# Kernel tuning notes

Measured on AMD Instinct MI355X. Metric: run time of the kernel, lower is better.

The kernel has to match this reference:

```python
import jax, jax.numpy as jnp
import numpy as np

WAYS, SHOTS = 32, 64
N = WAYS * SHOTS
XDIM, CIN = 84, 3
FLAT = 10 * 19 * 19  # 3610 after conv/pool stack
ZDIM = 2 * 32 * 4    # 256

def _conv2d(x, w, b):
    y = jax.lax.conv_general_dilated(x, w, (1, 1), 'VALID',
        dimension_numbers=('NCHW', 'OIHW', 'NCHW'))
    return y + b[None, :, None, None]

def _maxpool2(x):
    return jax.lax.reduce_window(x, -jnp.inf, jax.lax.max,
        (1, 1, 2, 2), (1, 1, 2, 2), 'VALID')

def setup_inputs() -> dict:
    key = jax.random.key(0)
    ks = jax.random.split(key, 32)
    rn = lambda k, shape, s=0.05: jax.random.normal(k, shape, jnp.float32) * s
    labels = jax.random.randint(ks[0], (N,), 0, WAYS)
    y = jax.nn.one_hot(labels, WAYS, dtype=jnp.float32)
    z = lambda n: jnp.zeros((n,), jnp.float32)
    return {
        'x': jax.random.normal(ks[1], (N, CIN, XDIM, XDIM), jnp.float32),
        'y': y,
        'conv1_w': rn(ks[2], (10, CIN, 3, 3)), 'conv1_b': z(10),
        'conv2_w': rn(ks[3], (10, 10, 3, 3)), 'conv2_b': z(10),
        'enc_w': rn(ks[4], (FLAT, 64)), 'enc_b': z(64),
        't1_w': rn(ks[5], (3, 4), 0.2), 't1_b': z(4),
        'te2_w1': rn(ks[6], (256, 128)), 'te2_b1': z(128),
        'te2_w2': rn(ks[7], (128, 32)), 'te2_b2': z(32),
        't2_w': rn(ks[8], (3, 4), 0.2), 't2_b': z(4),
        'om_mu_w': rn(ks[9], (256, 1)), 'om_mu_b': z(1),
        'om_sd_w': rn(ks[10], (256, 1)), 'om_sd_b': z(1),
        'ga_w': rn(ks[11], (128, 64)), 'ga_b': z(64),
        'ga_mu_w': rn(ks[12], (64, 5)), 'ga_mu_b': z(5),
        'ga_sd_w': rn(ks[13], (64, 5)), 'ga_sd_b': z(5),
        'ze_w': rn(ks[14], (128, 64)), 'ze_b': z(64),
        'ze_mu_w': rn(ks[15], (64, ZDIM)), 'ze_mu_b': z(ZDIM),
        'ze_sd_w': rn(ks[16], (64, ZDIM)), 'ze_sd_b': z(ZDIM),
        'do_sample': 0,
    }

def _kl_std_normal(mu, sigma):
    # KL(N(mu, sigma) || N(0, 1)), summed
    return jnp.sum(-jnp.log(sigma) + 0.5 * (sigma * sigma + mu * mu) - 0.5)

def _forward(x, y, conv1_w, conv1_b, conv2_w, conv2_b, enc_w, enc_b,
             t1_w, t1_b, te2_w1, te2_b1, te2_w2, te2_b2, t2_w, t2_b,
             om_mu_w, om_mu_b, om_sd_w, om_sd_b,
             ga_w, ga_b, ga_mu_w, ga_mu_b, ga_sd_w, ga_sd_b,
             ze_w, ze_b, ze_mu_w, ze_mu_b, ze_sd_w, ze_sd_b):
    relu = jax.nn.relu
    # class encoder: conv-relu-pool x2 + flatten + linear -> [N, 64]
    h = _maxpool2(relu(_conv2d(x, conv1_w, conv1_b)))
    h = _maxpool2(relu(_conv2d(h, conv2_w, conv2_b)))
    h = h.reshape(h.shape[0], -1) @ enc_w + enc_b  # [N, 64]
    # statistics_pooling_1: per-class masked var/mean/cardinality (vectorized over classes)
    y_sum = jnp.sum(y, axis=1)           # [N]
    y_arg = jnp.argmax(y, axis=1)        # [N]
    cls_mask = ((y_arg[None, :] == jnp.arange(WAYS)[:, None]) &
                (y_sum[None, :] > 0)).astype(jnp.float32)  # [W, N]
    xm = h[None, :, :] * cls_mask[:, :, None]              # [W, N, 64]
    mean = jnp.mean(xm, axis=1)                            # [W, 64]
    var = jnp.var(xm, axis=1, ddof=1)                      # unbiased, matches torch.var_mean
    card = (jnp.sum(y[None, :, :] * cls_mask[:, :, None], axis=(1, 2)) - 1.0) / (SHOTS - 1.0)  # [W]
    cs = jnp.stack([mean, var, jnp.broadcast_to(card[:, None], (WAYS, 64))], axis=2)  # [W, 64, 3]
    cs = relu(cs @ t1_w + t1_b).reshape(WAYS, -1)          # [W, 256]
    # statistics_pooling_2
    ts = relu(cs @ te2_w1 + te2_b1) @ te2_w2 + te2_b2      # [W, 32]
    t = jnp.stack([jnp.mean(ts, axis=0), jnp.var(ts, axis=0, ddof=1),
                   jnp.broadcast_to(jnp.sum(card), (32,))], axis=1)  # [32, 3]
    t = relu(t @ t2_w + t2_b).reshape(1, -1)               # [1, 128]
    # omega (use_s=True: heads applied to class_summary directly)
    mu_o = relu(cs @ om_mu_w + om_mu_b)[:, 0]              # [W]
    sd_o = jax.nn.softplus(relu(cs @ om_sd_w + om_sd_b)[:, 0])
    # gamma
    eg = relu(t @ ga_w + ga_b)                             # [1, 64]
    mu_g = relu(eg @ ga_mu_w + ga_mu_b)[0]                 # [5]
    sd_g = jax.nn.softplus(relu(eg @ ga_sd_w + ga_sd_b)[0])
    # zeta
    ez = relu(t @ ze_w + ze_b)                             # [1, 64]
    mu_z = relu(ez @ ze_mu_w + ze_mu_b)[0]                 # [256]
    sd_z = jax.nn.softplus(relu(ez @ ze_sd_w + ze_sd_b)[0])
    kl = _kl_std_normal(mu_o, sd_o) + _kl_std_normal(mu_g, sd_g) + _kl_std_normal(mu_z, sd_z)
    # deterministic path (do_sample=False -> distribution means); concat for a single output
    return jnp.concatenate([mu_o, mu_g, mu_z, kl[None]])   # [W + 5 + 256 + 1]

def reference(x, y, conv1_w, conv1_b, conv2_w, conv2_b, enc_w, enc_b,
              t1_w, t1_b, te2_w1, te2_b1, te2_w2, te2_b2, t2_w, t2_b,
              om_mu_w, om_mu_b, om_sd_w, om_sd_b,
              ga_w, ga_b, ga_mu_w, ga_mu_b, ga_sd_w, ga_sd_b,
              ze_w, ze_b, ze_mu_w, ze_mu_b, ze_sd_w, ze_sd_b, do_sample):
    return _forward(x, y, conv1_w, conv1_b, conv2_w, conv2_b, enc_w, enc_b,
                    t1_w, t1_b, te2_w1, te2_b1, te2_w2, te2_b2, t2_w, t2_b,
                    om_mu_w, om_mu_b, om_sd_w, om_sd_b,
                    ga_w, ga_b, ga_mu_w, ga_mu_b, ga_sd_w, ga_sd_b,
                    ze_w, ze_b, ze_mu_w, ze_mu_b, ze_sd_w, ze_sd_b)
```

## Files before the change

kernel.cpp:

```cpp
#include <hip/hip_runtime.h>
#include <math.h>

#define WAYS 32
#define NTOT 2048
#define XD 84
#define FLAT 3610
#define KSPLIT 16
#define KCHUNK 226

__device__ __forceinline__ float softplus_f(float x) {
    return (x > 20.f) ? x : log1pf(expf(x));
}
__device__ __forceinline__ float kl_f(float mu, float sd) {
    return -logf(sd) + 0.5f * (sd * sd + mu * mu) - 0.5f;
}

__global__ __launch_bounds__(256, 3) void k_conv(
        const float* __restrict__ x,
        const float* __restrict__ w1, const float* __restrict__ b1,
        const float* __restrict__ w2, const float* __restrict__ b2,
        float* __restrict__ p2) {
    __shared__ __align__(16) float xs[3 * 22 * 84];
    __shared__ __align__(16) float p1s[10 * 10 * 40];
    __shared__ __align__(16) float w1t[27 * 12];
    __shared__ __align__(16) float w2t[90 * 16];

    const int tid  = threadIdx.x;
    const int img  = blockIdx.x & 2047;
    const int band = blockIdx.x >> 11;
    const int r0   = band * 4;
    const int nr   = (band < 4) ? 4 : 3;
    const int nq   = 2 * nr + 2;
    const int xr0  = 16 * band;
    const int nxr  = 2 * nq + 2;

    {
        const float* xg = x + (size_t)img * (3 * XD * XD);
        const int nv = (nxr * 84) >> 2;
        #pragma unroll
        for (int c = 0; c < 3; c++) {
            const float4* src = (const float4*)(xg + c * (XD * XD) + xr0 * 84);
            float4* dst = (float4*)(xs + c * (22 * 84));
            for (int i = tid; i < nv; i += 256) dst[i] = src[i];
        }
    }
    for (int i = tid; i < 270; i += 256) {
        int oc = i / 27, r = i - oc * 27;
        w1t[r * 12 + oc] = w1[i];
    }
    for (int i = tid; i < 900; i += 256) {
        int oc = i / 90, r = i - oc * 90;
        int h = oc / 5, o = oc - h * 5;
        w2t[r * 16 + h * 8 + o] = w2[i];
    }
    float b1r[10];
    #pragma unroll
    for (int o = 0; o < 10; o++) b1r[o] = b1[o];
    __syncthreads();

    {
        const int n1 = nq * 40;
        #pragma unroll 1
        for (int it = tid; it < n1; it += 256) {
            asm volatile("" ::: "memory");
            int q = it / 40;
            int p = it - q * 40;
            float acc[10][4];
            #pragma unroll
            for (int o = 0; o < 10; o++)
                #pragma unroll
                for (int j = 0; j < 4; j++) acc[o][j] = 0.f;
            #pragma unroll 1
            for (int c = 0; c < 3; c++) {
                float xp[4][4];
                #pragma unroll
                for (int rr = 0; rr < 4; rr++) {
                    const float2* row =
                        (const float2*)&xs[c * (22 * 84) + (2 * q + rr) * 84 + 2 * p];
                    float2 lo = row[0], hi = row[1];
                    xp[rr][0] = lo.x; xp[rr][1] = lo.y;
                    xp[rr][2] = hi.x; xp[rr][3] = hi.y;
                }
                #pragma unroll
                for (int ky = 0; ky < 3; ky++) {
                    #pragma unroll
                    for (int kx = 0; kx < 3; kx++) {
                        const float* wr = &w1t[(c * 9 + ky * 3 + kx) * 12];
                        float4 wA = *(const float4*)(wr);
                        float4 wB = *(const float4*)(wr + 4);
                        float2 wC = *(const float2*)(wr + 8);
                        float wv[10] = {wA.x, wA.y, wA.z, wA.w,
                                        wB.x, wB.y, wB.z, wB.w,
                                        wC.x, wC.y};
                        #pragma unroll
                        for (int o = 0; o < 10; o++) {
                            float w = wv[o];
                            acc[o][0] = fmaf(xp[ky][kx],         w, acc[o][0]);
                            acc[o][1] = fmaf(xp[ky][kx + 1],     w, acc[o][1]);
                            acc[o][2] = fmaf(xp[ky + 1][kx],     w, acc[o][2]);
                            acc[o][3] = fmaf(xp[ky + 1][kx + 1], w, acc[o][3]);
                        }
                    }
                }
            }
            #pragma unroll
            for (int o = 0; o < 10; o++) {
                float m = fmaxf(fmaxf(acc[o][0], acc[o][1]), fmaxf(acc[o][2], acc[o][3]));
                p1s[o * 400 + q * 40 + p] = fmaxf(m + b1r[o], 0.f);
            }
        }
    }
    __syncthreads();

    {
        const int npos = nr * 19;
        if (tid < 152) {
            int half = (tid >= 76) ? 1 : 0;
            int pos  = tid - 76 * half;
            if (pos < npos) {
                int pr = pos / 19;
                int pc = pos - pr * 19;
                float acc[5][4];
                #pragma unroll
                for (int o = 0; o < 5; o++)
                    #pragma unroll
                    for (int j = 0; j < 4; j++) acc[o][j] = 0.f;
                #pragma unroll 1
                for (int ic = 0; ic < 10; ic++) {
                    float xp[4][4];
                    #pragma unroll
                    for (int rr = 0; rr < 4; rr++) {
                        const float2* row =
                            (const float2*)&p1s[ic * 400 + (2 * pr + rr) * 40 + 2 * pc];
                        float2 lo = row[0], hi = row[1];
                        xp[rr][0] = lo.x; xp[rr][1] = lo.y;
                        xp[rr][2] = hi.x; xp[rr][3] = hi.y;
                    }
                    #pragma unroll
                    for (int ky = 0; ky < 3; ky++) {
                        #pragma unroll
                        for (int kx = 0; kx < 3; kx++) {
                            const float* wr = &w2t[(ic * 9 + ky * 3 + kx) * 16 + half * 8];
                            float4 wA = *(const float4*)(wr);
                            float w4 = wr[4];
                            float wv[5] = {wA.x, wA.y, wA.z, wA.w, w4};
                            #pragma unroll
                            for (int o = 0; o < 5; o++) {
                                float w = wv[o];
                                acc[o][0] = fmaf(xp[ky][kx],         w, acc[o][0]);
                                acc[o][1] = fmaf(xp[ky][kx + 1],     w, acc[o][1]);
                                acc[o][2] = fmaf(xp[ky + 1][kx],     w, acc[o][2]);
                                acc[o][3] = fmaf(xp[ky + 1][kx + 1], w, acc[o][3]);
                            }
                        }
                    }
                }
                float* outp = p2 + (size_t)img * FLAT;
                #pragma unroll
                for (int o = 0; o < 5; o++) {
                    int oc = half * 5 + o;
                    float m = fmaxf(fmaxf(acc[o][0], acc[o][1]), fmaxf(acc[o][2], acc[o][3]));
                    outp[oc * 361 + (r0 + pr) * 19 + pc] = fmaxf(m + b2[oc], 0.f);
                }
            }
        }
    }
}

__global__ void k_label(const float* __restrict__ y, int* __restrict__ label) {
    int n = blockIdx.x * 256 + threadIdx.x;
    if (n >= NTOT) return;
    const float* yr = y + n * WAYS;
    float best = yr[0]; int bi = 0;
    for (int k = 1; k < WAYS; k++) {
        float v = yr[k];
        if (v > best) { best = v; bi = k; }
    }
    label[n] = bi;
}

__global__ __launch_bounds__(256, 2) void k_enc(
        const float* __restrict__ A, const float* __restrict__ W,
        float* __restrict__ H) {
    __shared__ float a_s[32 * 66];
    __shared__ float w_s[32 * 64];
    int mb = blockIdx.x >> 4;
    int ks = blockIdx.x & 15;
    int row0 = mb * 64;
    int kbeg = ks * KCHUNK;
    int kend = min(kbeg + KCHUNK, FLAT);
    int tid = threadIdx.x;
    int tr = tid & 15, tc = tid >> 4;
    float acc[4][4] = {};

    for (int k0 = kbeg; k0 < kend; k0 += 32) {
        {
            int kk = tid & 31;
            int r  = tid >> 5;
            int gk = k0 + kk;
            #pragma unroll
            for (int i = 0; i < 8; i++) {
                int rr = r + i * 8;
                float v = (gk < kend) ? A[(size_t)(row0 + rr) * FLAT + gk] : 0.f;
                a_s[kk * 66 + rr] = v;
            }
            int c  = tid & 63;
            int kw = tid >> 6;
            #pragma unroll
            for (int i = 0; i < 8; i++) {
                int kk2 = kw + i * 4;
                int gk2 = k0 + kk2;
                float v = (gk2 < kend) ? W[(size_t)gk2 * 64 + c] : 0.f;
                w_s[kk2 * 64 + c] = v;
            }
        }
        __syncthreads();
        #pragma unroll 8
        for (int k = 0; k < 32; k++) {
            float av[4], wv[4];
            #pragma unroll
            for (int i = 0; i < 4; i++) av[i] = a_s[k * 66 + tr * 4 + i];
            #pragma unroll
            for (int j = 0; j < 4; j++) wv[j] = w_s[k * 64 + tc * 4 + j];
            #pragma unroll
            for (int i = 0; i < 4; i++)
                #pragma unroll
                for (int j = 0; j < 4; j++)
                    acc[i][j] = fmaf(av[i], wv[j], acc[i][j]);
        }
        __syncthreads();
    }
    #pragma unroll
    for (int i = 0; i < 4; i++)
        #pragma unroll
        for (int j = 0; j < 4; j++)
            atomicAdd(&H[(size_t)(row0 + tr * 4 + i) * 64 + tc * 4 + j], acc[i][j]);
}

__global__ __launch_bounds__(1024) void k_stats(
        const float* __restrict__ H, const float* __restrict__ encb,
        const int* __restrict__ label,
        const float* __restrict__ t1w, const float* __restrict__ t1b,
        float* __restrict__ cs, float* __restrict__ card) {
    __shared__ int   lbl_s[NTOT];
    __shared__ float rs[16][64], rs2[16][64];
    __shared__ int rc[16];
    int w = blockIdx.x;
    int tid = threadIdx.x;
    for (int i = tid; i < NTOT; i += 1024) lbl_s[i] = label[i];
    __syncthreads();
    int c = tid & 63, g = tid >> 6;
    float eb = encb[c];
    float s = 0.f, s2 = 0.f; int cnt = 0;
    #pragma unroll 4
    for (int n = g; n < NTOT; n += 16) {
        bool m = (lbl_s[n] == w);
        float hv = H[n * 64 + c] + eb;
        float hm = m ? hv : 0.f;
        s += hm; s2 += hm * hm; cnt += m ? 1 : 0;
    }
    rs[g][c] = s; rs2[g][c] = s2;
    if (c == 0) rc[g] = cnt;
    __syncthreads();
    if (g == 0) {
        float S = 0.f, S2 = 0.f; int CNT = 0;
        #pragma unroll
        for (int gg = 0; gg < 16; gg++) {
            S += rs[gg][c]; S2 += rs2[gg][c]; CNT += rc[gg];
        }
        float mean = S / 2048.f;
        float var  = (S2 - S * S / 2048.f) / 2047.f;
        float cd   = ((float)CNT - 1.f) / 63.f;
        #pragma unroll
        for (int j = 0; j < 4; j++)
            cs[w * 256 + c * 4 + j] =
                fmaxf(mean * t1w[j] + var * t1w[4 + j] + cd * t1w[8 + j] + t1b[j], 0.f);
        if (c == 0) card[w] = cd;
    }
}

__global__ __launch_bounds__(256) void k_head(
        const float* __restrict__ cs_g, const float* __restrict__ card,
        const float* __restrict__ te2w1, const float* __restrict__ te2b1,
        const float* __restrict__ te2w2, const float* __restrict__ te2b2,
        const float* __restrict__ t2w, const float* __restrict__ t2b,
        const float* __restrict__ omw, const float* __restrict__ omb,
        const float* __restrict__ osw, const float* __restrict__ osb,
        const float* __restrict__ gaw, const float* __restrict__ gab,
        const float* __restrict__ gmw, const float* __restrict__ gmb,
        const float* __restrict__ gsw, const float* __restrict__ gsb,
        const float* __restrict__ zew, const float* __restrict__ zeb,
        const float* __restrict__ zmw, const float* __restrict__ zmb,
        const float* __restrict__ zsw, const float* __restrict__ zsb,
        float* __restrict__ out) {
    __shared__ float cst[256 * 36];
    __shared__ float a1t[128 * 36];
    __shared__ float ts[32 * 32];
    __shared__ float tv[128];
    __shared__ float eg_s[64], ez_s[64];
    __shared__ float red[256];
    int tid = threadIdx.x;

    for (int i = tid; i < 32 * 256; i += 256) {
        int w = i >> 8, k = i & 255;
        cst[k * 36 + w] = cs_g[i];
    }
    __syncthreads();

    {
        int wg = tid >> 5, jg = tid & 31;
        int w0 = wg * 4, j0 = jg * 4;
        float acc[4][4] = {};
        for (int k = 0; k < 256; k++) {
            float cva[4], wva[4];
            #pragma unroll
            for (int i = 0; i < 4; i++) cva[i] = cst[k * 36 + w0 + i];
            #pragma unroll
            for (int j = 0; j < 4; j++) wva[j] = te2w1[k * 128 + j0 + j];
            #pragma unroll
            for (int i = 0; i < 4; i++)
                #pragma unroll
                for (int j = 0; j < 4; j++)
                    acc[i][j] = fmaf(cva[i], wva[j], acc[i][j]);
        }
        #pragma unroll
        for (int jj = 0; jj < 4; jj++) {
            float b = te2b1[j0 + jj];
            #pragma unroll
            for (int i = 0; i < 4; i++)
                a1t[(j0 + jj) * 36 + w0 + i] = fmaxf(acc[i][jj] + b, 0.f);
        }
    }
    __syncthreads();

    {
        int wg = tid >> 4, jg = tid & 15;
        int w0 = wg * 2, j0 = jg * 2;
        float acc[2][2] = {};
        for (int k = 0; k < 128; k++) {
            float a0 = a1t[k * 36 + w0];
            float a1 = a1t[k * 36 + w0 + 1];
            float b0 = te2w2[k * 32 + j0];
            float b1v = te2w2[k * 32 + j0 + 1];
            acc[0][0] = fmaf(a0, b0, acc[0][0]);
            acc[0][1] = fmaf(a0, b1v, acc[0][1]);
            acc[1][0] = fmaf(a1, b0, acc[1][0]);
            acc[1][1] = fmaf(a1, b1v, acc[1][1]);
        }
        #pragma unroll
        for (int i = 0; i < 2; i++)
            #pragma unroll
            for (int j = 0; j < 2; j++)
                ts[(w0 + i) * 32 + (j0 + j)] = acc[i][j] + te2b2[j0 + j];
    }
    __syncthreads();

    float muo = 0.f, sdo = 1.f;
    if (tid < 32) {
        float csum = 0.f;
        for (int w2 = 0; w2 < 32; w2++) csum += card[w2];
        float s = 0.f, s2 = 0.f;
        for (int w2 = 0; w2 < 32; w2++) { float v = ts[w2 * 32 + tid]; s += v; s2 += v * v; }
        float m  = s / 32.f;
        float vv = (s2 - s * s / 32.f) / 31.f;
        #pragma unroll
        for (int j = 0; j < 4; j++)
            tv[tid * 4 + j] = fmaxf(m * t2w[j] + vv * t2w[4 + j] + csum * t2w[8 + j] + t2b[j], 0.f);
    } else if (tid < 64) {
        int w = tid - 32;
        float am = 0.f, as = 0.f;
        for (int k = 0; k < 256; k++) {
            float cv = cst[k * 36 + w];
            am = fmaf(cv, omw[k], am);
            as = fmaf(cv, osw[k], as);
        }
        muo = fmaxf(am + omb[0], 0.f);
        sdo = softplus_f(fmaxf(as + osb[0], 0.f));
        out[w] = muo;
    }
    __syncthreads();

    if (tid >= 64 && tid < 128) {
        int j = tid - 64;
        float ag = gab[j], az = zeb[j];
        for (int k = 0; k < 128; k++) {
            float t = tv[k];
            ag = fmaf(t, gaw[k * 64 + j], ag);
            az = fmaf(t, zew[k * 64 + j], az);
        }
        eg_s[j] = fmaxf(ag, 0.f);
        ez_s[j] = fmaxf(az, 0.f);
    }
    __syncthreads();

    float r = 0.f;
    {
        int j = tid;
        float am = zmb[j], as = zsb[j];
        for (int k = 0; k < 64; k++) {
            float e = ez_s[k];
            am = fmaf(e, zmw[k * 256 + j], am);
            as = fmaf(e, zsw[k * 256 + j], as);
        }
        float mu = fmaxf(am, 0.f);
        float sd = softplus_f(fmaxf(as, 0.f));
        out[37 + j] = mu;
        r += kl_f(mu, sd);
    }
    if (tid < 5) {
        float am = gmb[tid], as = gsb[tid];
        for (int k = 0; k < 64; k++) {
            float e = eg_s[k];
            am = fmaf(e, gmw[k * 5 + tid], am);
            as = fmaf(e, gsw[k * 5 + tid], as);
        }
        float mu = fmaxf(am, 0.f);
        float sd = softplus_f(fmaxf(as, 0.f));
        out[32 + tid] = mu;
        r += kl_f(mu, sd);
    }
    if (tid >= 32 && tid < 64) r += kl_f(muo, sdo);
    red[tid] = r;
    __syncthreads();
    for (int s = 128; s > 0; s >>= 1) {
        if (tid < s) red[tid] += red[tid + s];
        __syncthreads();
    }
    if (tid == 0) out[293] = red[0];
}

extern "C" void kernel_launch(void* const* d_in, const int* in_sizes, int n_in,
                              void* d_out, int out_size, void* d_ws, size_t ws_size,
                              hipStream_t stream) {
    const float* x    = (const float*)d_in[0];
    const float* y    = (const float*)d_in[1];
    const float* w1   = (const float*)d_in[2];
    const float* b1   = (const float*)d_in[3];
    const float* w2   = (const float*)d_in[4];
    const float* b2   = (const float*)d_in[5];
    const float* encw = (const float*)d_in[6];
    const float* encb = (const float*)d_in[7];
    const float* t1w  = (const float*)d_in[8];
    const float* t1b  = (const float*)d_in[9];
    const float* te2w1 = (const float*)d_in[10];
    const float* te2b1 = (const float*)d_in[11];
    const float* te2w2 = (const float*)d_in[12];
    const float* te2b2 = (const float*)d_in[13];
    const float* t2w  = (const float*)d_in[14];
    const float* t2b  = (const float*)d_in[15];
    const float* omw  = (const float*)d_in[16];
    const float* omb  = (const float*)d_in[17];
    const float* osw  = (const float*)d_in[18];
    const float* osb  = (const float*)d_in[19];
    const float* gaw  = (const float*)d_in[20];
    const float* gab  = (const float*)d_in[21];
    const float* gmw  = (const float*)d_in[22];
    const float* gmb  = (const float*)d_in[23];
    const float* gsw  = (const float*)d_in[24];
    const float* gsb  = (const float*)d_in[25];
    const float* zew  = (const float*)d_in[26];
    const float* zeb  = (const float*)d_in[27];
    const float* zmw  = (const float*)d_in[28];
    const float* zmb  = (const float*)d_in[29];
    const float* zsw  = (const float*)d_in[30];
    const float* zsb  = (const float*)d_in[31];
    float* out = (float*)d_out;

    float* p2   = (float*)d_ws;
    float* H    = p2 + (size_t)NTOT * FLAT;
    int*   lbl  = (int*)(H + NTOT * 64);
    float* cs   = (float*)(lbl + NTOT);
    float* card = cs + 32 * 256;

    hipMemsetAsync(H, 0, NTOT * 64 * sizeof(float), stream);
    hipLaunchKernelGGL(k_conv, dim3(NTOT * 5), dim3(256), 0, stream, x, w1, b1, w2, b2, p2);
    hipLaunchKernelGGL(k_label, dim3(8), dim3(256), 0, stream, y, lbl);
    hipLaunchKernelGGL(k_enc, dim3(32 * KSPLIT), dim3(256), 0, stream, p2, encw, H);
    hipLaunchKernelGGL(k_stats, dim3(32), dim3(1024), 0, stream, H, encb, lbl, t1w, t1b, cs, card);
    hipLaunchKernelGGL(k_head, dim3(1), dim3(256), 0, stream, cs, card,
                       te2w1, te2b1, te2w2, te2b2, t2w, t2b,
                       omw, omb, osw, osb, gaw, gab, gmw, gmb, gsw, gsb,
                       zew, zeb, zmw, zmb, zsw, zsb, out);
}
```

Before: 635.8 us.

## Alias conv1 output onto input smem buffer and split head reductions

The conv kernel now reuses the input tile's shared buffer for the pooled conv1 output. Each thread computes at most two conv1 items and holds them in registers until a barrier, then writes them back, so the separate p1s buffer is no longer needed. The smaller shared footprint allows launch bounds of 4 blocks per SM instead of 3. The head kernel vectorises its shared and global loads and spreads the omega and gamma/zeta dot products across all threads with a partial-sum reduction. This may raise register pressure in conv, and it relies on n1 never exceeding 512.

```diff
diff --git a/kernel.cpp b/kernel.cpp
--- a/kernel.cpp
+++ b/kernel.cpp
@@ -15,13 +15,14 @@
     return -logf(sd) + 0.5f * (sd * sd + mu * mu) - 0.5f;
 }
 
-__global__ __launch_bounds__(256, 3) void k_conv(
+struct Out10 { float v[10]; };
+
+__global__ __launch_bounds__(256, 4) void k_conv(
         const float* __restrict__ x,
         const float* __restrict__ w1, const float* __restrict__ b1,
         const float* __restrict__ w2, const float* __restrict__ b2,
         float* __restrict__ p2) {
-    __shared__ __align__(16) float xs[3 * 22 * 84];
-    __shared__ __align__(16) float p1s[10 * 10 * 40];
+    __shared__ __align__(16) float u_s[3 * 22 * 84];
     __shared__ __align__(16) float w1t[27 * 12];
     __shared__ __align__(16) float w2t[90 * 16];
 
@@ -40,7 +41,7 @@
         #pragma unroll
         for (int c = 0; c < 3; c++) {
             const float4* src = (const float4*)(xg + c * (XD * XD) + xr0 * 84);
-            float4* dst = (float4*)(xs + c * (22 * 84));
+            float4* dst = (float4*)(u_s + c * (22 * 84));
             for (int i = tid; i < nv; i += 256) dst[i] = src[i];
         }
     }
@@ -58,56 +59,76 @@
     for (int o = 0; o < 10; o++) b1r[o] = b1[o];
     __syncthreads();
 
-    {
-        const int n1 = nq * 40;
+    const int n1 = nq * 40;
+
+    auto conv1_item = [&](int q, int p) -> Out10 {
+        float acc[10][4];
+        #pragma unroll
+        for (int o = 0; o < 10; o++)
+            #pragma unroll
+            for (int j = 0; j < 4; j++) acc[o][j] = 0.f;
         #pragma unroll 1
-        for (int it = tid; it < n1; it += 256) {
-            asm volatile("" ::: "memory");
-            int q = it / 40;
-            int p = it - q * 40;
-            float acc[10][4];
-            #pragma unroll
-            for (int o = 0; o < 10; o++)
+        for (int c = 0; c < 3; c++) {
+            float xp[4][4];
+            #pragma unroll
+            for (int rr = 0; rr < 4; rr++) {
+                const float2* row =
+                    (const float2*)&u_s[c * (22 * 84) + (2 * q + rr) * 84 + 2 * p];
+                float2 lo = row[0], hi = row[1];
+                xp[rr][0] = lo.x; xp[rr][1] = lo.y;
+                xp[rr][2] = hi.x; xp[rr][3] = hi.y;
+            }
+            #pragma unroll
+            for (int ky = 0; ky < 3; ky++) {
                 #pragma unroll
-                for (int j = 0; j < 4; j++) acc[o][j] = 0.f;
-            #pragma unroll 1
-            for (int c = 0; c < 3; c++) {
-                float xp[4][4];
-                #pragma unroll
-                for (int rr = 0; rr < 4; rr++) {
-                    const float2* row =
-                        (const float2*)&xs[c * (22 * 84) + (2 * q + rr) * 84 + 2 * p];
-                    float2 lo = row[0], hi = row[1];
-                    xp[rr][0] = lo.x; xp[rr][1] = lo.y;
-                    xp[rr][2] = hi.x; xp[rr][3] = hi.y;
-                }
-                #pragma unroll
-                for (int ky = 0; ky < 3; ky++) {
+                for (int kx = 0; kx < 3; kx++) {
+                    const float* wr = &w1t[(c * 9 + ky * 3 + kx) * 12];
+                    float4 wA = *(const float4*)(wr);
+                    float4 wB = *(const float4*)(wr + 4);
+                    float2 wC = *(const float2*)(wr + 8);
+                    float wv[10] = {wA.x, wA.y, wA.z, wA.w,
+                                    wB.x, wB.y, wB.z, wB.w,
+                                    wC.x, wC.y};
                     #pragma unroll
-                    for (int kx = 0; kx < 3; kx++) {
-                        const float* wr = &w1t[(c * 9 + ky * 3 + kx) * 12];
-                        float4 wA = *(const float4*)(wr);
-                        float4 wB = *(const float4*)(wr + 4);
-                        float2 wC = *(const float2*)(wr + 8);
-                        float wv[10] = {wA.x, wA.y, wA.z, wA.w,
-                                        wB.x, wB.y, wB.z, wB.w,
-                                        wC.x, wC.y};
-                        #pragma unroll
-                        for (int o = 0; o < 10; o++) {
-                            float w = wv[o];
-                            acc[o][0] = fmaf(xp[ky][kx],         w, acc[o][0]);
-                            acc[o][1] = fmaf(xp[ky][kx + 1],     w, acc[o][1]);
-                            acc[o][2] = fmaf(xp[ky + 1][kx],     w, acc[o][2]);
-                            acc[o][3] = fmaf(xp[ky + 1][kx + 1], w, acc[o][3]);
-                        }
+                    for (int o = 0; o < 10; o++) {
+                        float w = wv[o];
+                        acc[o][0] = fmaf(xp[ky][kx],         w, acc[o][0]);
+                        acc[o][1] = fmaf(xp[ky][kx + 1],     w, acc[o][1]);
+                        acc[o][2] = fmaf(xp[ky + 1][kx],     w, acc[o][2]);
+                        acc[o][3] = fmaf(xp[ky + 1][kx + 1], w, acc[o][3]);
                     }
                 }
             }
-            #pragma unroll
-            for (int o = 0; o < 10; o++) {
-                float m = fmaxf(fmaxf(acc[o][0], acc[o][1]), fmaxf(acc[o][2], acc[o][3]));
-                p1s[o * 400 + q * 40 + p] = fmaxf(m + b1r[o], 0.f);
-            }
+        }
+        Out10 r;
+        #pragma unroll
+        for (int o = 0; o < 10; o++) {
+            float m = fmaxf(fmaxf(acc[o][0], acc[o][1]), fmaxf(acc[o][2], acc[o][3]));
+            r.v[o] = fmaxf(m + b1r[o], 0.f);
+        }
+        return r;
+    };
+
+    Out10 A, B;
+    {
+        int q = tid / 40, p = tid - q * 40;
+        A = conv1_item(q, p);
+    }
+    asm volatile("" ::: "memory");
+    const int itB = tid + 256;
+    const bool hasB = (itB < n1);
+    if (hasB) {
+        int q = itB / 40, p = itB - q * 40;
+        B = conv1_item(q, p);
+    }
+    __syncthreads();
+
+    {
+        #pragma unroll
+        for (int o = 0; o < 10; o++) u_s[o * 400 + tid] = A.v[o];
+        if (hasB) {
+            #pragma unroll
+            for (int o = 0; o < 10; o++) u_s[o * 400 + itB] = B.v[o];
         }
     }
     __syncthreads();
@@ -131,7 +152,7 @@
                     #pragma unroll
                     for (int rr = 0; rr < 4; rr++) {
                         const float2* row =
-                            (const float2*)&p1s[ic * 400 + (2 * pr + rr) * 40 + 2 * pc];
+                            (const float2*)&u_s[ic * 400 + (2 * pr + rr) * 40 + 2 * pc];
                         float2 lo = row[0], hi = row[1];
                         xp[rr][0] = lo.x; xp[rr][1] = lo.y;
                         xp[rr][2] = hi.x; xp[rr][3] = hi.y;
@@ -293,12 +314,13 @@
         const float* __restrict__ zmw, const float* __restrict__ zmb,
         const float* __restrict__ zsw, const float* __restrict__ zsb,
         float* __restrict__ out) {
-    __shared__ float cst[256 * 36];
-    __shared__ float a1t[128 * 36];
+    __shared__ __align__(16) float cst[256 * 36];
+    __shared__ __align__(16) float a1t[128 * 36];
     __shared__ float ts[32 * 32];
     __shared__ float tv[128];
     __shared__ float eg_s[64], ez_s[64];
     __shared__ float red[256];
+    __shared__ float redb[512];
     int tid = threadIdx.x;
 
     for (int i = tid; i < 32 * 256; i += 256) {
@@ -312,11 +334,10 @@
         int w0 = wg * 4, j0 = jg * 4;
         float acc[4][4] = {};
         for (int k = 0; k < 256; k++) {
-            float cva[4], wva[4];
-            #pragma unroll
-            for (int i = 0; i < 4; i++) cva[i] = cst[k * 36 + w0 + i];
-            #pragma unroll
-            for (int j = 0; j < 4; j++) wva[j] = te2w1[k * 128 + j0 + j];
+            float4 cv4 = *(const float4*)&cst[k * 36 + w0];
+            float4 wv4 = *(const float4*)&te2w1[k * 128 + j0];
+            float cva[4] = {cv4.x, cv4.y, cv4.z, cv4.w};
+            float wva[4] = {wv4.x, wv4.y, wv4.z, wv4.w};
             #pragma unroll
             for (int i = 0; i < 4; i++)
                 #pragma unroll
@@ -338,14 +359,12 @@
         int w0 = wg * 2, j0 = jg * 2;
         float acc[2][2] = {};
         for (int k = 0; k < 128; k++) {
-            float a0 = a1t[k * 36 + w0];
-            float a1 = a1t[k * 36 + w0 + 1];
-            float b0 = te2w2[k * 32 + j0];
-            float b1v = te2w2[k * 32 + j0 + 1];
-            acc[0][0] = fmaf(a0, b0, acc[0][0]);
-            acc[0][1] = fmaf(a0, b1v, acc[0][1]);
-            acc[1][0] = fmaf(a1, b0, acc[1][0]);
-            acc[1][1] = fmaf(a1, b1v, acc[1][1]);
+            float2 a2 = *(const float2*)&a1t[k * 36 + w0];
+            float2 b2v = *(const float2*)&te2w2[k * 32 + j0];
+            acc[0][0] = fmaf(a2.x, b2v.x, acc[0][0]);
+            acc[0][1] = fmaf(a2.x, b2v.y, acc[0][1]);
+            acc[1][0] = fmaf(a2.y, b2v.x, acc[1][0]);
+            acc[1][1] = fmaf(a2.y, b2v.y, acc[1][1]);
         }
         #pragma unroll
         for (int i = 0; i < 2; i++)
@@ -353,43 +372,70 @@
             for (int j = 0; j < 2; j++)
                 ts[(w0 + i) * 32 + (j0 + j)] = acc[i][j] + te2b2[j0 + j];
     }
+
+    {
+        int w = tid & 31, part = tid >> 5;
+        int k0 = part * 32;
+        float am = 0.f, as = 0.f;
+        #pragma unroll 4
+        for (int k = k0; k < k0 + 32; k++) {
+            float cv = cst[k * 36 + w];
+            am = fmaf(cv, omw[k], am);
+            as = fmaf(cv, osw[k], as);
+        }
+        redb[part * 32 + w] = am;
+        redb[256 + part * 32 + w] = as;
+    }
     __syncthreads();
 
     float muo = 0.f, sdo = 1.f;
     if (tid < 32) {
+        float am = 0.f, as = 0.f;
+        #pragma unroll
+        for (int p = 0; p < 8; p++) {
+            am += redb[p * 32 + tid];
+            as += redb[256 + p * 32 + tid];
+        }
+        muo = fmaxf(am + omb[0], 0.f);
+        sdo = softplus_f(fmaxf(as + osb[0], 0.f));
+        out[tid] = muo;
+    } else if (tid < 64) {
+        int t_ = tid - 32;
         float csum = 0.f;
         for (int w2 = 0; w2 < 32; w2++) csum += card[w2];
         float s = 0.f, s2 = 0.f;
-        for (int w2 = 0; w2 < 32; w2++) { float v = ts[w2 * 32 + tid]; s += v; s2 += v * v; }
+        for (int w2 = 0; w2 < 32; w2++) { float v = ts[w2 * 32 + t_]; s += v; s2 += v * v; }
         float m  = s / 32.f;
         float vv = (s2 - s * s / 32.f) / 31.f;
         #pragma unroll
         for (int j = 0; j < 4; j++)
-            tv[tid * 4 + j] = fmaxf(m * t2w[j] + vv * t2w[4 + j] + csum * t2w[8 + j] + t2b[j], 0.f);
-    } else if (tid < 64) {
-        int w = tid - 32;
-        float am = 0.f, as = 0.f;
-        for (int k = 0; k < 256; k++) {
-            float cv = cst[k * 36 + w];
-            am = fmaf(cv, omw[k], am);
-            as = fmaf(cv, osw[k], as);
-        }
-        muo = fmaxf(am + omb[0], 0.f);
-        sdo = softplus_f(fmaxf(as + osb[0], 0.f));
-        out[w] = muo;
-    }
-    __syncthreads();
-
-    if (tid >= 64 && tid < 128) {
-        int j = tid - 64;
-        float ag = gab[j], az = zeb[j];
-        for (int k = 0; k < 128; k++) {
+            tv[t_ * 4 + j] = fmaxf(m * t2w[j] + vv * t2w[4 + j] + csum * t2w[8 + j] + t2b[j], 0.f);
+    }
+    __syncthreads();
+
+    {
+        int j = tid & 63, part = tid >> 6;
+        int k0 = part * 32;
+        float ag = 0.f, az = 0.f;
+        #pragma unroll 4
+        for (int k = k0; k < k0 + 32; k++) {
             float t = tv[k];
             ag = fmaf(t, gaw[k * 64 + j], ag);
             az = fmaf(t, zew[k * 64 + j], az);
         }
-        eg_s[j] = fmaxf(ag, 0.f);
-        ez_s[j] = fmaxf(az, 0.f);
+        redb[part * 64 + j] = ag;
+        redb[256 + part * 64 + j] = az;
+    }
+    __syncthreads();
+    if (tid < 64) {
+        float ag = gab[tid], az = zeb[tid];
+        #pragma unroll
+        for (int p = 0; p < 4; p++) {
+            ag += redb[p * 64 + tid];
+            az += redb[256 + p * 64 + tid];
+        }
+        eg_s[tid] = fmaxf(ag, 0.f);
+        ez_s[tid] = fmaxf(az, 0.f);
     }
     __syncthreads();
 
@@ -419,7 +465,7 @@
         out[32 + tid] = mu;
         r += kl_f(mu, sd);
     }
-    if (tid >= 32 && tid < 64) r += kl_f(muo, sdo);
+    if (tid < 32) r += kl_f(muo, sdo);
     red[tid] = r;
     __syncthreads();
     for (int s = 128; s > 0; s >>= 1) {
```

After: 641.8 us. About the same (+1.0%).
